# Kernel tuning notes

Hardware: AMD Instinct MI355X
Metric: run time of the kernel (lower is better)

The kernel has to match this reference:

```python
import jax, jax.numpy as jnp
import numpy as np

DIM = 128      # token feature dim
HEADS = 4
HEAD_DIM = DIM // HEADS
H = 512
W = 512
NSP = 4096     # n_spixels = H*W/scale
TEMP = DIM ** (-0.5)   # NOTE: original scales by full-dim ** -0.5
NEG = -9.0e15
EPS = 1e-12    # torch F.normalize eps


def setup_inputs() -> dict:
    key = jax.random.key(0)
    k1, k2, k3, k4 = jax.random.split(key, 4)
    return {
        "spf": jax.random.normal(k1, (DIM, NSP), jnp.float32),
        "segments": jax.random.randint(k2, (H, W), 0, NSP, jnp.int32),
        "w_qkv": jax.random.normal(k3, (DIM, 3 * DIM), jnp.float32) / np.sqrt(DIM),
        "w_out": jax.random.normal(k4, (DIM, DIM), jnp.float32) / np.sqrt(DIM),
        "b_out": jnp.zeros((DIM,), jnp.float32),
    }


def build_adjacency(seg, n_sp):
    """Vectorized version of get_A: for every 2x2 window (i in [0,h-3], j in [0,w-3])
    connect the max and min superpixel labels; zero the diagonal."""
    a = seg[:-2, :-2]
    b = seg[:-2, 1:-1]
    c = seg[1:-1, :-2]
    d = seg[1:-1, 1:-1]
    mx = jnp.maximum(jnp.maximum(a, b), jnp.maximum(c, d)).ravel()
    mn = jnp.minimum(jnp.minimum(a, b), jnp.minimum(c, d)).ravel()
    A = jnp.zeros((n_sp, n_sp), jnp.float32)
    A = A.at[mx, mn].set(1.0)
    A = A.at[mn, mx].set(1.0)
    # fill_diagonal(A, 0) (also removes windows where max == min)
    A = A * (1.0 - jnp.eye(n_sp, dtype=jnp.float32))
    return A


def _l2norm(t):
    n = jnp.sqrt(jnp.sum(t * t, axis=-1, keepdims=True))
    return t / jnp.maximum(n, EPS)


def reference(spf, segments, w_qkv, w_out, b_out):
    A = build_adjacency(segments, NSP)                      # [n, n]
    x = spf.T                                               # [n, dim]
    qkv = x @ w_qkv                                         # [n, 3*dim]
    q, k, v = jnp.split(qkv, 3, axis=-1)
    split = lambda t: t.reshape(NSP, HEADS, HEAD_DIM).transpose(1, 0, 2)  # [h, n, d]
    q, k, v = split(q), split(k), split(v)
    q = _l2norm(q)
    k = _l2norm(k)
    # Original masks per-head scores, then keeps only head 0's attention
    # (attn[0][0]) and broadcasts it over all heads' v. We compute only
    # head 0's scores (mathematically identical output).
    scores = (q[0] @ k[0].T) * TEMP                         # [n, n] cosine scores
    scores = jnp.where(A > 0, scores, NEG)
    eye = jnp.eye(NSP, dtype=bool)
    scores = jnp.where(eye, 1.0, scores)                    # np.fill_diagonal(attn, 1)
    attn = jax.nn.softmax(scores, axis=-1)                  # [n, n]
    out = jnp.einsum('nm,hmd->hnd', attn, v)                # shared attn over heads
    out = out.transpose(1, 0, 2).reshape(NSP, DIM)          # [n, dim]
    out = out @ w_out + b_out                               # to_out Linear
    # map_sp2p: scatter superpixel features back to pixel grid (hard assignment)
    pix = out[segments]                                     # [H, W, dim]
    return pix.transpose(2, 0, 1)[None]                     # [1, dim, H, W]
```

## Files before the change

### kernel.cpp

```cpp
#include <hip/hip_runtime.h>

#define NSP 4096
#define HW 512
#define TEMP 0.08838834764831845f
#define MAXE 640
#define PREP_ZERO 512
#define PREP_WF 64
#define ADJ_BLOCKS 1017
#define QKV_BLOCKS 768

__global__ void __launch_bounds__(256) prep(
    unsigned int* __restrict__ mask, const float* __restrict__ wqkv,
    const float* __restrict__ wout, float* __restrict__ Wf) {
    int t = threadIdx.x;
    if (blockIdx.x < PREP_ZERO) {
        ((uint4*)mask)[blockIdx.x * 256 + t] = make_uint4(0u, 0u, 0u, 0u);
        return;
    }
    int gid = (blockIdx.x - PREP_ZERO) * 256 + t;
    int d = gid >> 7, c = gid & 127;
    float acc = 0.f;
#pragma unroll 8
    for (int k = 0; k < 128; ++k)
        acc += wqkv[d * 384 + 256 + k] * wout[k * 128 + c];
    Wf[d * 128 + c] = acc;
}

__global__ void __launch_bounds__(256) adj_qkv(
    const int* __restrict__ seg, unsigned int* __restrict__ mask,
    const float* __restrict__ spf, const float* __restrict__ wqkv,
    const float* __restrict__ Wf,
    float* __restrict__ Q0, float* __restrict__ K0, float* __restrict__ V) {
    int t = threadIdx.x;
    if (blockIdx.x < ADJ_BLOCKS) {
        int idx = blockIdx.x * 256 + t;
        if (idx >= 510 * 510) return;
        int i = idx / 510, j = idx - i * 510;
        const int* r = seg + i * HW + j;
        int a = r[0], b = r[1], c = r[HW], d = r[HW + 1];
        int mx = max(max(a, b), max(c, d));
        int mn = min(min(a, b), min(c, d));
        if (mx == mn) return;
        atomicOr(&mask[mx * 128 + (mn >> 5)], 1u << (mn & 31));
        atomicOr(&mask[mn * 128 + (mx >> 5)], 1u << (mx & 31));
        return;
    }
    int gid = (blockIdx.x - ADJ_BLOCKS) * 256 + t;
    int g = gid % 48;
    int n = gid / 48;
    const float* wbase;
    int wstride;
    float* outp;
    if (g < 8)       { wbase = wqkv + g * 4;               wstride = 384; outp = Q0 + n * 32  + g * 4; }
    else if (g < 16) { wbase = wqkv + 128 + (g - 8) * 4;   wstride = 384; outp = K0 + n * 32  + (g - 8) * 4; }
    else             { wbase = Wf + (g - 16) * 4;          wstride = 128; outp = V  + n * 128 + (g - 16) * 4; }
    float4 acc = {0.f, 0.f, 0.f, 0.f};
#pragma unroll 8
    for (int d = 0; d < 128; ++d) {
        float x = spf[d * NSP + n];
        float4 w = *(const float4*)(wbase + d * wstride);
        acc.x += x * w.x; acc.y += x * w.y; acc.z += x * w.z; acc.w += x * w.w;
    }
    if (g < 16) {
        float s = acc.x * acc.x + acc.y * acc.y + acc.z * acc.z + acc.w * acc.w;
        s += __shfl_xor(s, 1);
        s += __shfl_xor(s, 2);
        s += __shfl_xor(s, 4);
        float inv = 1.0f / fmaxf(sqrtf(s), 1e-12f);
        acc.x *= inv; acc.y *= inv; acc.z *= inv; acc.w *= inv;
    }
    *(float4*)outp = acc;
}

__global__ void __launch_bounds__(128) sparse_attn(
    const unsigned int* __restrict__ mask, const float* __restrict__ Q0,
    const float* __restrict__ K0, const float* __restrict__ V,
    const float* __restrict__ bout, float* __restrict__ final) {
    int n = blockIdx.x;
    int t = threadIdx.x;
    int lane = t & 63, wid = t >> 6;
    __shared__ unsigned int words[128];
    __shared__ int   pfx[128];
    __shared__ int   midx[MAXE];
    __shared__ float wts[MAXE];
    __shared__ float q0s[32];
    __shared__ float4 redv[4][32];
    __shared__ float  redw[4];

    unsigned int w = mask[n * 128 + t];
    words[t] = w;
    if (t < 32) q0s[t] = Q0[n * 32 + t];

    int p = __popc(w);
#pragma unroll
    for (int off = 1; off < 64; off <<= 1) {
        int y = __shfl_up(p, off);
        if (lane >= off) p += y;
    }
    pfx[t] = p;
    __syncthreads();
    if (wid == 1) pfx[t] = p + pfx[63];
    __syncthreads();
    int E = min(pfx[127], MAXE);

    for (int e = t; e < E; e += 128) {
        int lo = 0, hi = 127;
        while (lo < hi) { int mid = (lo + hi) >> 1; if (pfx[mid] > e) hi = mid; else lo = mid + 1; }
        int base = (lo > 0) ? pfx[lo - 1] : 0;
        int r = e - base;
        unsigned int x = words[lo];
        for (int i = 0; i < r; ++i) x &= x - 1;
        int m = lo * 32 + (__ffs(x) - 1);
        const float4* kp = (const float4*)(K0 + m * 32);
        float s = 0.f;
#pragma unroll
        for (int i = 0; i < 8; ++i) {
            float4 kv = kp[i];
            s += q0s[i * 4 + 0] * kv.x + q0s[i * 4 + 1] * kv.y +
                 q0s[i * 4 + 2] * kv.z + q0s[i * 4 + 3] * kv.w;
        }
        wts[e]  = __expf(s * TEMP - 1.0f);
        midx[e] = m;
    }
    __syncthreads();

    int cg = t & 31, eg = t >> 5;
    const float4* V4 = (const float4*)V;
    float4 acc = {0.f, 0.f, 0.f, 0.f};
    float wp = 0.f;
    int e = eg;
    for (; e + 4 < E; e += 8) {
        float wa = wts[e];     int ma = midx[e];
        float wb = wts[e + 4]; int mb = midx[e + 4];
        float4 va = V4[ma * 32 + cg];
        float4 vb = V4[mb * 32 + cg];
        acc.x += wa * va.x + wb * vb.x;
        acc.y += wa * va.y + wb * vb.y;
        acc.z += wa * va.z + wb * vb.z;
        acc.w += wa * va.w + wb * vb.w;
        wp += wa + wb;
    }
    for (; e < E; e += 4) {
        float wt = wts[e];
        float4 v = V4[midx[e] * 32 + cg];
        acc.x += wt * v.x; acc.y += wt * v.y; acc.z += wt * v.z; acc.w += wt * v.w;
        wp += wt;
    }
    redv[eg][cg] = acc;
    if (cg == 0) redw[eg] = wp;
    __syncthreads();
    if (t < 32) {
        float4 a0 = redv[0][t], a1 = redv[1][t], a2 = redv[2][t], a3 = redv[3][t];
        float ws = 1.0f + redw[0] + redw[1] + redw[2] + redw[3];
        float4 vd = V4[n * 32 + t];
        float4 bb = ((const float4*)bout)[t];
        float inv = 1.0f / ws;
        float4 o;
        o.x = (a0.x + a1.x + a2.x + a3.x + vd.x) * inv + bb.x;
        o.y = (a0.y + a1.y + a2.y + a3.y + vd.y) * inv + bb.y;
        o.z = (a0.z + a1.z + a2.z + a3.z + vd.z) * inv + bb.z;
        o.w = (a0.w + a1.w + a2.w + a3.w + vd.w) * inv + bb.w;
        ((float4*)final)[n * 32 + t] = o;
    }
}

#define GT_PIX 64
__global__ void __launch_bounds__(256) gather_out(
    const float* __restrict__ final, const int* __restrict__ seg,
    float* __restrict__ out) {
    __shared__ __align__(16) float tile[GT_PIX][132];
    __shared__ int sseg[GT_PIX];
    int base = blockIdx.x * GT_PIX;
    int t = threadIdx.x;
    if (t < GT_PIX) sseg[t] = seg[base + t];
    __syncthreads();

    int c4 = t & 31, pp = t >> 5;
    const float4* f4 = (const float4*)final;
#pragma unroll
    for (int i = 0; i < 8; ++i) {
        int p = pp + 8 * i;
        float4 v = f4[sseg[p] * 32 + c4];
        *(float4*)&tile[p][c4 * 4] = v;
    }
    __syncthreads();

    int jp = t >> 4;
    int cg = t & 15;
#pragma unroll
    for (int pass = 0; pass < 8; ++pass) {
        int cc = cg + 16 * pass;
        float4 v;
        v.x = tile[4 * jp + 0][cc];
        v.y = tile[4 * jp + 1][cc];
        v.z = tile[4 * jp + 2][cc];
        v.w = tile[4 * jp + 3][cc];
        *(float4*)(out + (size_t)cc * (HW * HW) + base + 4 * jp) = v;
    }
}

extern "C" void kernel_launch(void* const* d_in, const int* in_sizes, int n_in,
                              void* d_out, int out_size, void* d_ws, size_t ws_size,
                              hipStream_t stream) {
    const float* spf  = (const float*)d_in[0];
    const int*   seg  = (const int*)d_in[1];
    const float* wqkv = (const float*)d_in[2];
    const float* wout = (const float*)d_in[3];
    const float* bout = (const float*)d_in[4];
    float* out = (float*)d_out;

    char* ws = (char*)d_ws;
    unsigned int* mask = (unsigned int*)ws;
    float* Q0    = (float*)(ws + (2u << 20));
    float* K0    = (float*)(ws + (2u << 20) + (512u << 10));
    float* V     = (float*)(ws + (3u << 20));
    float* final = (float*)(ws + (5u << 20));
    float* Wf    = (float*)(ws + (7u << 20));

    hipLaunchKernelGGL(prep, dim3(PREP_ZERO + PREP_WF), dim3(256), 0, stream,
                       mask, wqkv, wout, Wf);
    hipLaunchKernelGGL(adj_qkv, dim3(ADJ_BLOCKS + QKV_BLOCKS), dim3(256), 0, stream,
                       seg, mask, spf, wqkv, Wf, Q0, K0, V);
    hipLaunchKernelGGL(sparse_attn, dim3(4096), dim3(128), 0, stream,
                       mask, Q0, K0, V, bout, final);
    hipLaunchKernelGGL(gather_out, dim3((HW * HW) / GT_PIX), dim3(256), 0, stream,
                       final, seg, out);
}
```

Baseline: 215.3 us.

## Fuse four kernel launches into one cooperative persistent kernel with grid syncs

Merges the prep, adjacency/QKV, sparse attention and gather stages into a single cooperative kernel of 1024 blocks that separates phases with grid.sync(). Each block handles two superpixels per attention pass and walks the gather work in strides. The aim is to remove launch gaps and inter-kernel drain/fill. The cost is a fixed grid and grid-wide barriers, shared memory sized to the largest phase (two attention states), and possibly lower occupancy. If the cooperative launch fails, the code falls back to the old four-kernel path.

```diff
diff --git a/kernel.cpp b/kernel.cpp
--- a/kernel.cpp
+++ b/kernel.cpp
@@ -1,9 +1,208 @@
 #include <hip/hip_runtime.h>
-
-#define NSP 4096
-#define HW 512
-#define TEMP 0.08838834764831845f
-#define MAXE 640
+#include <hip/hip_cooperative_groups.h>
+
+namespace cg = cooperative_groups;
+
+#define NSP   4096
+#define HW    512
+#define TEMP  0.08838834764831845f
+#define MAXE  640
+#define GRID  1024
+#define NTHR  256
+#define TOTT  (GRID * NTHR)
+
+struct AttnS {
+    unsigned int words[128];
+    int   pfx[128];
+    int   midx[MAXE];
+    float wts[MAXE];
+    float q0s[32];
+    float4 redv[4][32];
+    float redw[4];
+};
+struct GathS {
+    float tile[32][132];
+    int   sseg[32];
+};
+constexpr size_t SMEM_BYTES = (2 * sizeof(AttnS) > sizeof(GathS)) ? 2 * sizeof(AttnS) : sizeof(GathS);
+
+__global__ void __launch_bounds__(NTHR, 4) fused_all(
+    const int* __restrict__ seg, const float* __restrict__ spf,
+    const float* __restrict__ wqkv, const float* __restrict__ wout,
+    const float* __restrict__ bout, float* __restrict__ out,
+    unsigned int* __restrict__ mask, float* __restrict__ Q0,
+    float* __restrict__ K0, float* __restrict__ Vp,
+    float* __restrict__ fin, float* __restrict__ Wf)
+{
+    cg::grid_group grid = cg::this_grid();
+    __shared__ __align__(16) char smem[SMEM_BYTES];
+    const int t   = threadIdx.x;
+    const int tid = blockIdx.x * NTHR + t;
+
+    if (tid < 131072) {
+        ((uint4*)mask)[tid] = make_uint4(0u, 0u, 0u, 0u);
+    } else if (tid < 147456) {
+        int gid = tid - 131072;
+        int d = gid >> 7, c = gid & 127;
+        float acc = 0.f;
+#pragma unroll 8
+        for (int k = 0; k < 128; ++k)
+            acc += wqkv[d * 384 + 256 + k] * wout[k * 128 + c];
+        Wf[d * 128 + c] = acc;
+    }
+    grid.sync();
+
+    for (int vt = tid; vt < 456708; vt += TOTT) {
+        if (vt < 196608) {
+            int g = vt % 48, n = vt / 48;
+            const float* wbase; int wstride; float* outp;
+            if (g < 8)       { wbase = wqkv + g * 4;             wstride = 384; outp = Q0 + n * 32  + g * 4; }
+            else if (g < 16) { wbase = wqkv + 128 + (g - 8) * 4; wstride = 384; outp = K0 + n * 32  + (g - 8) * 4; }
+            else             { wbase = Wf + (g - 16) * 4;        wstride = 128; outp = Vp + n * 128 + (g - 16) * 4; }
+            float4 acc = {0.f, 0.f, 0.f, 0.f};
+#pragma unroll 8
+            for (int d = 0; d < 128; ++d) {
+                float x = spf[d * NSP + n];
+                float4 w = *(const float4*)(wbase + d * wstride);
+                acc.x += x * w.x; acc.y += x * w.y; acc.z += x * w.z; acc.w += x * w.w;
+            }
+            if (g < 16) {
+                float s = acc.x * acc.x + acc.y * acc.y + acc.z * acc.z + acc.w * acc.w;
+                s += __shfl_xor(s, 1); s += __shfl_xor(s, 2); s += __shfl_xor(s, 4);
+                float inv = 1.0f / fmaxf(sqrtf(s), 1e-12f);
+                acc.x *= inv; acc.y *= inv; acc.z *= inv; acc.w *= inv;
+            }
+            *(float4*)outp = acc;
+        } else {
+            int aid = vt - 196608;
+            int i = aid / 510, j = aid - i * 510;
+            const int* r = seg + i * HW + j;
+            int a = r[0], b = r[1], c = r[HW], d = r[HW + 1];
+            int mx = max(max(a, b), max(c, d));
+            int mn = min(min(a, b), min(c, d));
+            if (mx != mn) {
+                atomicOr(&mask[mx * 128 + (mn >> 5)], 1u << (mn & 31));
+                atomicOr(&mask[mn * 128 + (mx >> 5)], 1u << (mx & 31));
+            }
+        }
+    }
+    grid.sync();
+
+    for (int it = 0; it < 2; ++it) {
+        if (it) __syncthreads();
+        AttnS* A = ((AttnS*)smem) + (t >> 7);
+        const int tt   = t & 127;
+        const int n    = it * 2048 + blockIdx.x * 2 + (t >> 7);
+        const int lane = t & 63;
+        const int wid  = tt >> 6;
+
+        unsigned int w = mask[n * 128 + tt];
+        A->words[tt] = w;
+        if (tt < 32) A->q0s[tt] = Q0[n * 32 + tt];
+        int p = __popc(w);
+#pragma unroll
+        for (int off = 1; off < 64; off <<= 1) {
+            int y = __shfl_up(p, off);
+            if (lane >= off) p += y;
+        }
+        A->pfx[tt] = p;
+        __syncthreads();
+        if (wid == 1) A->pfx[tt] = p + A->pfx[63];
+        __syncthreads();
+        int E = min(A->pfx[127], MAXE);
+
+        for (int e = tt; e < E; e += 128) {
+            int lo = 0, hi = 127;
+            while (lo < hi) { int mid = (lo + hi) >> 1; if (A->pfx[mid] > e) hi = mid; else lo = mid + 1; }
+            int base = lo ? A->pfx[lo - 1] : 0;
+            int r = e - base;
+            unsigned int x = A->words[lo];
+            for (int i = 0; i < r; ++i) x &= x - 1;
+            int m = lo * 32 + (__ffs(x) - 1);
+            const float4* kp = (const float4*)(K0 + m * 32);
+            float s = 0.f;
+#pragma unroll
+            for (int i = 0; i < 8; ++i) {
+                float4 kv = kp[i];
+                s += A->q0s[i * 4 + 0] * kv.x + A->q0s[i * 4 + 1] * kv.y +
+                     A->q0s[i * 4 + 2] * kv.z + A->q0s[i * 4 + 3] * kv.w;
+            }
+            A->wts[e]  = __expf(s * TEMP - 1.0f);
+            A->midx[e] = m;
+        }
+        __syncthreads();
+
+        int cg_ = tt & 31, eg = tt >> 5;
+        const float4* V4 = (const float4*)Vp;
+        float4 acc = {0.f, 0.f, 0.f, 0.f};
+        float wp = 0.f;
+        int e = eg;
+        for (; e + 4 < E; e += 8) {
+            float wa = A->wts[e];     int ma = A->midx[e];
+            float wb = A->wts[e + 4]; int mb = A->midx[e + 4];
+            float4 va = V4[ma * 32 + cg_];
+            float4 vb = V4[mb * 32 + cg_];
+            acc.x += wa * va.x + wb * vb.x; acc.y += wa * va.y + wb * vb.y;
+            acc.z += wa * va.z + wb * vb.z; acc.w += wa * va.w + wb * vb.w;
+            wp += wa + wb;
+        }
+        for (; e < E; e += 4) {
+            float wt = A->wts[e];
+            float4 v = V4[A->midx[e] * 32 + cg_];
+            acc.x += wt * v.x; acc.y += wt * v.y; acc.z += wt * v.z; acc.w += wt * v.w;
+            wp += wt;
+        }
+        A->redv[eg][cg_] = acc;
+        if (cg_ == 0) A->redw[eg] = wp;
+        __syncthreads();
+        if (tt < 32) {
+            float4 a0 = A->redv[0][tt], a1 = A->redv[1][tt], a2 = A->redv[2][tt], a3 = A->redv[3][tt];
+            float wsum = 1.0f + A->redw[0] + A->redw[1] + A->redw[2] + A->redw[3];
+            float4 vd = V4[n * 32 + tt];
+            float4 bb = ((const float4*)bout)[tt];
+            float inv = 1.0f / wsum;
+            float4 o;
+            o.x = (a0.x + a1.x + a2.x + a3.x + vd.x) * inv + bb.x;
+            o.y = (a0.y + a1.y + a2.y + a3.y + vd.y) * inv + bb.y;
+            o.z = (a0.z + a1.z + a2.z + a3.z + vd.z) * inv + bb.z;
+            o.w = (a0.w + a1.w + a2.w + a3.w + vd.w) * inv + bb.w;
+            ((float4*)fin)[n * 32 + tt] = o;
+        }
+        __syncthreads();
+    }
+    grid.sync();
+
+    {
+        GathS* G = (GathS*)smem;
+        const float4* f4 = (const float4*)fin;
+        for (int it = 0; it < 8; ++it) {
+            int base = (it * GRID + blockIdx.x) * 32;
+            if (it) __syncthreads();
+            if (t < 32) G->sseg[t] = seg[base + t];
+            __syncthreads();
+            int c4 = t & 31, pr = t >> 5;
+#pragma unroll
+            for (int i = 0; i < 4; ++i) {
+                int p = pr + 8 * i;
+                float4 v = f4[G->sseg[p] * 32 + c4];
+                *(float4*)&G->tile[p][c4 * 4] = v;
+            }
+            __syncthreads();
+            int i4 = t & 7, ccb = t >> 3;
+#pragma unroll
+            for (int pass = 0; pass < 4; ++pass) {
+                int cc = ccb + 32 * pass;
+                float4 v;
+                v.x = G->tile[4 * i4 + 0][cc];
+                v.y = G->tile[4 * i4 + 1][cc];
+                v.z = G->tile[4 * i4 + 2][cc];
+                v.w = G->tile[4 * i4 + 3][cc];
+                *(float4*)(out + (size_t)cc * (HW * HW) + base + 4 * i4) = v;
+            }
+        }
+    }
+}
+
 #define PREP_ZERO 512
 #define PREP_WF 64
 #define ADJ_BLOCKS 1017
@@ -48,9 +247,7 @@
     int gid = (blockIdx.x - ADJ_BLOCKS) * 256 + t;
     int g = gid % 48;
     int n = gid / 48;
-    const float* wbase;
-    int wstride;
-    float* outp;
+    const float* wbase; int wstride; float* outp;
     if (g < 8)       { wbase = wqkv + g * 4;               wstride = 384; outp = Q0 + n * 32  + g * 4; }
     else if (g < 16) { wbase = wqkv + 128 + (g - 8) * 4;   wstride = 384; outp = K0 + n * 32  + (g - 8) * 4; }
     else             { wbase = Wf + (g - 16) * 4;          wstride = 128; outp = V  + n * 128 + (g - 16) * 4; }
@@ -63,9 +260,7 @@
     }
     if (g < 16) {
         float s = acc.x * acc.x + acc.y * acc.y + acc.z * acc.z + acc.w * acc.w;
-        s += __shfl_xor(s, 1);
-        s += __shfl_xor(s, 2);
-        s += __shfl_xor(s, 4);
+        s += __shfl_xor(s, 1); s += __shfl_xor(s, 2); s += __shfl_xor(s, 4);
         float inv = 1.0f / fmaxf(sqrtf(s), 1e-12f);
         acc.x *= inv; acc.y *= inv; acc.z *= inv; acc.w *= inv;
     }
@@ -90,7 +285,6 @@
     unsigned int w = mask[n * 128 + t];
     words[t] = w;
     if (t < 32) q0s[t] = Q0[n * 32 + t];
-
     int p = __popc(w);
 #pragma unroll
     for (int off = 1; off < 64; off <<= 1) {
@@ -106,7 +300,7 @@
     for (int e = t; e < E; e += 128) {
         int lo = 0, hi = 127;
         while (lo < hi) { int mid = (lo + hi) >> 1; if (pfx[mid] > e) hi = mid; else lo = mid + 1; }
-        int base = (lo > 0) ? pfx[lo - 1] : 0;
+        int base = lo ? pfx[lo - 1] : 0;
         int r = e - base;
         unsigned int x = words[lo];
         for (int i = 0; i < r; ++i) x &= x - 1;
@@ -124,7 +318,7 @@
     }
     __syncthreads();
 
-    int cg = t & 31, eg = t >> 5;
+    int cg_ = t & 31, eg = t >> 5;
     const float4* V4 = (const float4*)V;
     float4 acc = {0.f, 0.f, 0.f, 0.f};
     float wp = 0.f;
@@ -132,29 +326,27 @@
     for (; e + 4 < E; e += 8) {
         float wa = wts[e];     int ma = midx[e];
         float wb = wts[e + 4]; int mb = midx[e + 4];
-        float4 va = V4[ma * 32 + cg];
-        float4 vb = V4[mb * 32 + cg];
-        acc.x += wa * va.x + wb * vb.x;
-        acc.y += wa * va.y + wb * vb.y;
-        acc.z += wa * va.z + wb * vb.z;
-        acc.w += wa * va.w + wb * vb.w;
+        float4 va = V4[ma * 32 + cg_];
+        float4 vb = V4[mb * 32 + cg_];
+        acc.x += wa * va.x + wb * vb.x; acc.y += wa * va.y + wb * vb.y;
+        acc.z += wa * va.z + wb * vb.z; acc.w += wa * va.w + wb * vb.w;
         wp += wa + wb;
     }
     for (; e < E; e += 4) {
         float wt = wts[e];
-        float4 v = V4[midx[e] * 32 + cg];
+        float4 v = V4[midx[e] * 32 + cg_];
         acc.x += wt * v.x; acc.y += wt * v.y; acc.z += wt * v.z; acc.w += wt * v.w;
         wp += wt;
     }
-    redv[eg][cg] = acc;
-    if (cg == 0) redw[eg] = wp;
+    redv[eg][cg_] = acc;
+    if (cg_ == 0) redw[eg] = wp;
     __syncthreads();
     if (t < 32) {
         float4 a0 = redv[0][t], a1 = redv[1][t], a2 = redv[2][t], a3 = redv[3][t];
-        float ws = 1.0f + redw[0] + redw[1] + redw[2] + redw[3];
+        float wsum = 1.0f + redw[0] + redw[1] + redw[2] + redw[3];
         float4 vd = V4[n * 32 + t];
         float4 bb = ((const float4*)bout)[t];
-        float inv = 1.0f / ws;
+        float inv = 1.0f / wsum;
         float4 o;
         o.x = (a0.x + a1.x + a2.x + a3.x + vd.x) * inv + bb.x;
         o.y = (a0.y + a1.y + a2.y + a3.y + vd.y) * inv + bb.y;
@@ -174,7 +366,6 @@
     int t = threadIdx.x;
     if (t < GT_PIX) sseg[t] = seg[base + t];
     __syncthreads();
-
     int c4 = t & 31, pp = t >> 5;
     const float4* f4 = (const float4*)final;
 #pragma unroll
@@ -184,12 +375,11 @@
         *(float4*)&tile[p][c4 * 4] = v;
     }
     __syncthreads();
-
     int jp = t >> 4;
-    int cg = t & 15;
+    int cg_ = t & 15;
 #pragma unroll
     for (int pass = 0; pass < 8; ++pass) {
-        int cc = cg + 16 * pass;
+        int cc = cg_ + 16 * pass;
         float4 v;
         v.x = tile[4 * jp + 0][cc];
         v.y = tile[4 * jp + 1][cc];
@@ -211,18 +401,30 @@
 
     char* ws = (char*)d_ws;
     unsigned int* mask = (unsigned int*)ws;
-    float* Q0    = (float*)(ws + (2u << 20));
-    float* K0    = (float*)(ws + (2u << 20) + (512u << 10));
-    float* V     = (float*)(ws + (3u << 20));
-    float* final = (float*)(ws + (5u << 20));
-    float* Wf    = (float*)(ws + (7u << 20));
-
-    hipLaunchKernelGGL(prep, dim3(PREP_ZERO + PREP_WF), dim3(256), 0, stream,
-                       mask, wqkv, wout, Wf);
-    hipLaunchKernelGGL(adj_qkv, dim3(ADJ_BLOCKS + QKV_BLOCKS), dim3(256), 0, stream,
-                       seg, mask, spf, wqkv, Wf, Q0, K0, V);
-    hipLaunchKernelGGL(sparse_attn, dim3(4096), dim3(128), 0, stream,
-                       mask, Q0, K0, V, bout, final);
-    hipLaunchKernelGGL(gather_out, dim3((HW * HW) / GT_PIX), dim3(256), 0, stream,
-                       final, seg, out);
-}
+    float* Q0  = (float*)(ws + (2u << 20));
+    float* K0  = (float*)(ws + (2u << 20) + (512u << 10));
+    float* Vp  = (float*)(ws + (3u << 20));
+    float* fin = (float*)(ws + (5u << 20));
+    float* Wf  = (float*)(ws + (7u << 20));
+
+    void* args[12];
+    args[0] = (void*)&seg;  args[1] = (void*)&spf;  args[2] = (void*)&wqkv;
+    args[3] = (void*)&wout; args[4] = (void*)&bout; args[5] = (void*)&out;
+    args[6] = (void*)&mask; args[7] = (void*)&Q0;   args[8] = (void*)&K0;
+    args[9] = (void*)&Vp;   args[10] = (void*)&fin; args[11] = (void*)&Wf;
+
+    hipError_t err = hipLaunchCooperativeKernel((const void*)fused_all,
+                                                dim3(GRID), dim3(NTHR),
+                                                args, 0, stream);
+    if (err != hipSuccess) {
+        (void)hipGetLastError();
+        hipLaunchKernelGGL(prep, dim3(PREP_ZERO + PREP_WF), dim3(256), 0, stream,
+                           mask, wqkv, wout, Wf);
+        hipLaunchKernelGGL(adj_qkv, dim3(ADJ_BLOCKS + QKV_BLOCKS), dim3(256), 0, stream,
+                           seg, mask, spf, wqkv, Wf, Q0, K0, Vp);
+        hipLaunchKernelGGL(sparse_attn, dim3(4096), dim3(128), 0, stream,
+                           mask, Q0, K0, Vp, bout, fin);
+        hipLaunchKernelGGL(gather_out, dim3((HW * HW) / GT_PIX), dim3(256), 0, stream,
+                           fin, seg, out);
+    }
+}
```

New measurement: 528.6 us. 146% more time.
